# Performance work log

Hardware: AMD Instinct MI355X
Metric: run time of the kernel (lower is better)

Reference implementation:

```python
import jax, jax.numpy as jnp
import numpy as np

B = 8192
IN = 2048   # input_size
H = 2048    # hidden_size
D = IN + H  # combine feature dim = 4096


def setup_inputs() -> dict:
    key = jax.random.key(0)
    ks = jax.random.split(key, 11)
    s = 1.0 / np.sqrt(D)  # nn.Linear default init scale
    inp = {
        "input": jax.random.normal(ks[0], (B, D), jnp.float32),
        "hidden": jax.random.normal(ks[1], (B, D), jnp.float32),
        "cell": jax.random.normal(ks[2], (B, H), jnp.float32),
        "Wf": jax.random.uniform(ks[3], (D, H), jnp.float32, -s, s),
        "bf": jax.random.uniform(ks[4], (H,), jnp.float32, -s, s),
        "Wc": jax.random.uniform(ks[5], (D, H), jnp.float32, -s, s),
        "bc": jax.random.uniform(ks[6], (H,), jnp.float32, -s, s),
        "Wi": jax.random.uniform(ks[7], (D, H), jnp.float32, -s, s),
        "bi": jax.random.uniform(ks[8], (H,), jnp.float32, -s, s),
        "Wo": jax.random.uniform(ks[9], (D, H), jnp.float32, -s, s),
        "bo": jax.random.uniform(ks[10], (H,), jnp.float32, -s, s),
    }
    return inp


def reference(input, hidden, cell, Wf, bf, Wc, bc, Wi, bi, Wo, bo):
    combine = input + hidden  # [B, D] elementwise add (as in source, not concat)
    # Fuse the 4 gate GEMMs into one [D, 4H] GEMM for efficiency (same math).
    W = jnp.concatenate([Wf, Wc, Wi, Wo], axis=1)  # [D, 4H]
    b = jnp.concatenate([bf, bc, bi, bo])          # [4H]
    gates = combine @ W + b                        # [B, 4H]
    gf, gc, gi, go = jnp.split(gates, 4, axis=1)
    ft = jax.nn.sigmoid(gf)
    ct_ = jnp.tanh(gc)
    it = jax.nn.sigmoid(jax.nn.sigmoid(gi))  # double sigmoid, faithful to source
    cell_state = cell * ft + ct_ * it
    out = jax.nn.sigmoid(go)
    hidden_state = out * jnp.tanh(cell_state)
    return (out, hidden_state, cell_state)
```

## Files before the change

### kernel.cpp

```cpp
#include <hip/hip_runtime.h>
#include <hip/hip_bf16.h>

#define B_SZ 8192
#define D_SZ 4096
#define H_SZ 2048
#define N4H  8192
#define NT   (D_SZ / 64)

typedef __attribute__((ext_vector_type(8))) __bf16 bf16x8;
typedef __attribute__((ext_vector_type(4))) float f32x4;

#define GPTR(p) ((__attribute__((address_space(1))) void*)(p))
#define LPTR(p) ((__attribute__((address_space(3))) void*)(p))

__global__ void combine_k(const float* __restrict__ x, const float* __restrict__ h,
                          __hip_bfloat16* __restrict__ c) {
    const size_t n4 = (size_t)B_SZ * D_SZ / 4;
    const size_t stride = (size_t)gridDim.x * blockDim.x;
    for (size_t i = (size_t)blockIdx.x * blockDim.x + threadIdx.x; i < n4; i += stride) {
        float4 a = ((const float4*)x)[i];
        float4 b = ((const float4*)h)[i];
        short4 r;
        r.x = __builtin_bit_cast(short, __float2bfloat16(a.x + b.x));
        r.y = __builtin_bit_cast(short, __float2bfloat16(a.y + b.y));
        r.z = __builtin_bit_cast(short, __float2bfloat16(a.z + b.z));
        r.w = __builtin_bit_cast(short, __float2bfloat16(a.w + b.w));
        ((short4*)c)[i] = r;
    }
}

__global__ void transpose_w_k(const float* __restrict__ Wf, const float* __restrict__ Wc,
                              const float* __restrict__ Wi, const float* __restrict__ Wo,
                              __hip_bfloat16* __restrict__ WT) {
    __shared__ float t[32][33];
    const int k0 = blockIdx.x * 32;
    const int n0 = blockIdx.y * 32;
    const float* W = (n0 < H_SZ) ? Wf : (n0 < 2 * H_SZ) ? Wc : (n0 < 3 * H_SZ) ? Wi : Wo;
    const int nc = n0 & (H_SZ - 1);
    const int tx = threadIdx.x, ty = threadIdx.y;
#pragma unroll
    for (int j = 0; j < 4; ++j)
        t[ty + j * 8][tx] = W[(size_t)(k0 + ty + j * 8) * H_SZ + nc + tx];
    __syncthreads();
#pragma unroll
    for (int j = 0; j < 4; ++j)
        WT[(size_t)(n0 + ty + j * 8) * D_SZ + k0 + tx] = __float2bfloat16(t[tx][ty + j * 8]);
}


#define BAR()                                    \
    do {                                         \
        asm volatile("" ::: "memory");           \
        __builtin_amdgcn_s_barrier();            \
        asm volatile("" ::: "memory");           \
    } while (0)

#define STAGE(pbase, HSTRIDE, h, kt, region)                                           \
    do {                                                                               \
        __builtin_amdgcn_global_load_lds(                                              \
            GPTR((pbase) + (size_t)((h) * (HSTRIDE)) * D_SZ + (size_t)(kt) * 64),      \
            LPTR(smem + (region) + (h) * 16384 + wave * 1024), 16, 0, 0);              \
        __builtin_amdgcn_global_load_lds(                                              \
            GPTR((pbase) + (size_t)(128 + (h) * (HSTRIDE)) * D_SZ + (size_t)(kt) * 64),\
            LPTR(smem + (region) + (h) * 16384 + 8192 + wave * 1024), 16, 0, 0);       \
    } while (0)

#define LDA(dst, base, qm)                                                             \
    do {                                                                               \
        _Pragma("unroll") for (int mi = 0; mi < 4; ++mi) {                             \
            const int row_ = (qm) * 128 + wr * 64 + mi * 16 + fr;                      \
            dst[mi][0] = *(const bf16x8*)(smem + (base) + row_ * 128 + sw0);           \
            dst[mi][1] = *(const bf16x8*)(smem + (base) + row_ * 128 + sw1);           \
        }                                                                              \
    } while (0)

#define LDB(dst, base, qn)                                                             \
    do {                                                                               \
        _Pragma("unroll") for (int nf = 0; nf < 2; ++nf) {                             \
            const int row_ = (qn) * 128 + wc * 32 + nf * 16 + fr;                      \
            dst[nf][0] = *(const bf16x8*)(smem + (base) + row_ * 128 + sw0);           \
            dst[nf][1] = *(const bf16x8*)(smem + (base) + row_ * 128 + sw1);           \
        }                                                                              \
    } while (0)

#define MFMA_Q(qm, qn, areg, breg)                                                     \
    do {                                                                               \
        _Pragma("unroll") for (int mi = 0; mi < 4; ++mi)                               \
        _Pragma("unroll") for (int nf = 0; nf < 2; ++nf)                               \
        _Pragma("unroll") for (int ks = 0; ks < 2; ++ks)                               \
            acc[(qm) * 4 + mi][(qn) * 2 + nf] =                                        \
                __builtin_amdgcn_mfma_f32_16x16x32_bf16(                               \
                    areg[mi][ks], breg[nf][ks],                                        \
                    acc[(qm) * 4 + mi][(qn) * 2 + nf], 0, 0, 0);                       \
    } while (0)

__global__ __launch_bounds__(512, 2) void gemm8_k(
    const __hip_bfloat16* __restrict__ A,
    const __hip_bfloat16* __restrict__ BT,
    __hip_bfloat16* __restrict__ C)
{
    extern __shared__ char smem[];

    const int tid  = threadIdx.x;
    const int wave = tid >> 6;
    const int lane = tid & 63;
    const int wr = wave >> 2;
    const int wc = wave & 3;
    const int fr = lane & 15;
    const int sw0 = (((lane >> 4) + 0) ^ (fr & 7)) << 4;
    const int sw1 = (((lane >> 4) + 4) ^ (fr & 7)) << 4;

    const int wg = (blockIdx.x & 7) * 128 + (blockIdx.x >> 3);
    const int n0 = (wg & 31) * 256;
    const int m0 = (wg >> 5) * 256;

    const int r0   = tid >> 3;
    const int col0 = ((tid & 7) ^ (r0 & 7)) << 3;
    const __hip_bfloat16* pA = A  + (size_t)(m0 + r0) * D_SZ + col0;
    const __hip_bfloat16* pB = BT + (size_t)(n0 + ((r0 >> 5) << 6) + (r0 & 31)) * D_SZ + col0;

    f32x4 acc[8][4] = {};
    bf16x8 a[4][2], b0[2][2], b1[2][2];

    STAGE(pA, 64, 0, 0, 0);
    STAGE(pB, 32, 0, 0, 32768);
    STAGE(pA, 64, 1, 0, 0);
    STAGE(pB, 32, 1, 0, 32768);
    STAGE(pA, 64, 0, 1, 65536);
    STAGE(pB, 32, 0, 1, 98304);
    STAGE(pA, 64, 1, 1, 65536);
    asm volatile("s_waitcnt vmcnt(6)" ::: "memory");
    BAR();

    for (int t = 0; t < NT; ++t) {
        const int curA = (t & 1) * 65536;
        const int curB = curA + 32768;
        const int othB = (curA ^ 65536) + 32768;

        LDA(a, curA, 0);
        LDB(b0, curB, 0);
        if (t + 1 < NT) STAGE(pB, 32, 1, t + 1, othB);
        BAR();
        asm volatile("s_waitcnt lgkmcnt(0)" ::: "memory");
        __builtin_amdgcn_s_setprio(1);
        MFMA_Q(0, 0, a, b0);
        __builtin_amdgcn_s_setprio(0);
        BAR();

        LDB(b1, curB, 1);
        if (t + 2 < NT) STAGE(pA, 64, 0, t + 2, curA);
        BAR();
        asm volatile("s_waitcnt lgkmcnt(0)" ::: "memory");
        __builtin_amdgcn_s_setprio(1);
        MFMA_Q(0, 1, a, b1);
        __builtin_amdgcn_s_setprio(0);
        BAR();

        LDA(a, curA, 1);
        if (t + 2 < NT) STAGE(pB, 32, 0, t + 2, curB);
        BAR();
        asm volatile("s_waitcnt lgkmcnt(0)" ::: "memory");
        __builtin_amdgcn_s_setprio(1);
        MFMA_Q(1, 0, a, b0);
        __builtin_amdgcn_s_setprio(0);
        BAR();

        if (t + 2 < NT) STAGE(pA, 64, 1, t + 2, curA);
        BAR();
        __builtin_amdgcn_s_setprio(1);
        MFMA_Q(1, 1, a, b1);
        __builtin_amdgcn_s_setprio(0);
        if (t + 2 < NT) {
            asm volatile("s_waitcnt vmcnt(6)" ::: "memory");
        } else if (t + 1 < NT) {
            asm volatile("s_waitcnt vmcnt(0)" ::: "memory");
        }
        BAR();
    }

    const int crow = (lane >> 4) * 4;
    const int ccol = lane & 15;
#pragma unroll
    for (int ai = 0; ai < 8; ++ai)
#pragma unroll
        for (int bj = 0; bj < 4; ++bj) {
            const size_t base_r = (size_t)(m0 + wr * 128 + ai * 16 + crow);
            const size_t cidx   = (size_t)(n0 + wc * 64 + bj * 16 + ccol);
#pragma unroll
            for (int j = 0; j < 4; ++j)
                C[(base_r + j) * (size_t)N4H + cidx] = __float2bfloat16(acc[ai][bj][j]);
        }
}

__device__ __forceinline__ float bfbits(unsigned v, int j) {
    return __uint_as_float(j ? (v & 0xffff0000u) : (v << 16));
}
__device__ __forceinline__ float fsig(float x) { return 1.f / (1.f + __expf(-x)); }
__device__ __forceinline__ float ftanh(float x) {
    x = fminf(fmaxf(x, -15.f), 15.f);
    float e = __expf(2.f * x);
    return (e - 1.f) / (e + 1.f);
}

__global__ void gates_k(const __hip_bfloat16* __restrict__ g, const float* __restrict__ cell,
                        const float* __restrict__ bfb, const float* __restrict__ bcb,
                        const float* __restrict__ bib, const float* __restrict__ bob,
                        float* __restrict__ out) {
    const size_t BH = (size_t)B_SZ * H_SZ;
    float* hid = out + BH;
    float* cst = out + 2 * BH;
    const size_t n2 = BH / 2;
    const size_t stride = (size_t)gridDim.x * blockDim.x;
    for (size_t i = (size_t)blockIdx.x * blockDim.x + threadIdx.x; i < n2; i += stride) {
        const size_t e = i * 2;
        const int b = (int)(e >> 11);
        const int n = (int)(e & 2047);
        const unsigned* row = (const unsigned*)(g + (size_t)b * N4H);
        const unsigned vf = row[(n) >> 1];
        const unsigned vc = row[(n + 2048) >> 1];
        const unsigned vi = row[(n + 4096) >> 1];
        const unsigned vo = row[(n + 6144) >> 1];
        const float2 cl = *(const float2*)(cell + e);
        const float2 b_f = *(const float2*)(bfb + n);
        const float2 b_c = *(const float2*)(bcb + n);
        const float2 b_i = *(const float2*)(bib + n);
        const float2 b_o = *(const float2*)(bob + n);
        float r_out[2], r_hid[2], r_cst[2];
#pragma unroll
        for (int j = 0; j < 2; ++j) {
            const float gf = bfbits(vf, j) + (j ? b_f.y : b_f.x);
            const float gc = bfbits(vc, j) + (j ? b_c.y : b_c.x);
            const float gi = bfbits(vi, j) + (j ? b_i.y : b_i.x);
            const float go = bfbits(vo, j) + (j ? b_o.y : b_o.x);
            const float ft = fsig(gf);
            const float ct = ftanh(gc);
            const float it = fsig(fsig(gi));
            const float ot = fsig(go);
            const float cv = (j ? cl.y : cl.x);
            const float cs = cv * ft + ct * it;
            r_out[j] = ot;
            r_cst[j] = cs;
            r_hid[j] = ot * ftanh(cs);
        }
        *(float2*)(out + e) = make_float2(r_out[0], r_out[1]);
        *(float2*)(hid + e) = make_float2(r_hid[0], r_hid[1]);
        *(float2*)(cst + e) = make_float2(r_cst[0], r_cst[1]);
    }
}

extern "C" void kernel_launch(void* const* d_in, const int* in_sizes, int n_in,
                              void* d_out, int out_size, void* d_ws, size_t ws_size,
                              hipStream_t stream) {
    const float* input  = (const float*)d_in[0];
    const float* hidden = (const float*)d_in[1];
    const float* cell   = (const float*)d_in[2];
    const float* Wf     = (const float*)d_in[3];
    const float* bfb    = (const float*)d_in[4];
    const float* Wc     = (const float*)d_in[5];
    const float* bcb    = (const float*)d_in[6];
    const float* Wi     = (const float*)d_in[7];
    const float* bib    = (const float*)d_in[8];
    const float* Wo     = (const float*)d_in[9];
    const float* bob    = (const float*)d_in[10];
    float* out = (float*)d_out;

    char* ws = (char*)d_ws;
    __hip_bfloat16* comb  = (__hip_bfloat16*)ws;
    __hip_bfloat16* WT    = (__hip_bfloat16*)(ws + (size_t)B_SZ * D_SZ * 2);
    __hip_bfloat16* gates = (__hip_bfloat16*)(ws + (size_t)B_SZ * D_SZ * 2
                                                 + (size_t)N4H * D_SZ * 2);

    hipFuncSetAttribute(reinterpret_cast<const void*>(gemm8_k),
                        hipFuncAttributeMaxDynamicSharedMemorySize, 131072);

    combine_k<<<2048, 256, 0, stream>>>(input, hidden, comb);
    transpose_w_k<<<dim3(D_SZ / 32, N4H / 32), dim3(32, 8), 0, stream>>>(Wf, Wc, Wi, Wo, WT);
    gemm8_k<<<1024, 512, 131072, stream>>>(comb, WT, gates);
    gates_k<<<2048, 256, 0, stream>>>(gates, cell, bfb, bcb, bib, bob, out);
}
```

Baseline: 674.8 us.

## Fuse LSTM gate epilogue into GEMM via interleaved weight layout; merge prep kernels

The weight transpose now interleaves the four gates in groups of 16 columns, so each wave's 64-column tile holds the f/c/i/o values for the same 16 hidden units. That lets the GEMM epilogue apply the bias, activations and cell update directly from the accumulators, which removes the bf16 gates buffer round-trip and the separate gates kernel. The combine and transpose kernels are merged into one launch, nontemporal loads and stores are added, and the main loop is unrolled by two with constant buffer offsets. In exchange, the epilogue writes are scattered 4-byte stores and the cell reads are uncoalesced strided accesses, and the extra work may raise register pressure.

```diff
diff --git a/kernel.cpp b/kernel.cpp
--- a/kernel.cpp
+++ b/kernel.cpp
@@ -13,38 +13,46 @@
 #define GPTR(p) ((__attribute__((address_space(1))) void*)(p))
 #define LPTR(p) ((__attribute__((address_space(3))) void*)(p))
 
-__global__ void combine_k(const float* __restrict__ x, const float* __restrict__ h,
-                          __hip_bfloat16* __restrict__ c) {
-    const size_t n4 = (size_t)B_SZ * D_SZ / 4;
-    const size_t stride = (size_t)gridDim.x * blockDim.x;
-    for (size_t i = (size_t)blockIdx.x * blockDim.x + threadIdx.x; i < n4; i += stride) {
-        float4 a = ((const float4*)x)[i];
-        float4 b = ((const float4*)h)[i];
-        short4 r;
-        r.x = __builtin_bit_cast(short, __float2bfloat16(a.x + b.x));
-        r.y = __builtin_bit_cast(short, __float2bfloat16(a.y + b.y));
-        r.z = __builtin_bit_cast(short, __float2bfloat16(a.z + b.z));
-        r.w = __builtin_bit_cast(short, __float2bfloat16(a.w + b.w));
-        ((short4*)c)[i] = r;
-    }
-}
-
-__global__ void transpose_w_k(const float* __restrict__ Wf, const float* __restrict__ Wc,
-                              const float* __restrict__ Wi, const float* __restrict__ Wo,
-                              __hip_bfloat16* __restrict__ WT) {
+__global__ void prep_k(const float* __restrict__ x, const float* __restrict__ h,
+                       __hip_bfloat16* __restrict__ comb,
+                       const float* __restrict__ Wf, const float* __restrict__ Wc,
+                       const float* __restrict__ Wi, const float* __restrict__ Wo,
+                       __hip_bfloat16* __restrict__ WT) {
     __shared__ float t[32][33];
-    const int k0 = blockIdx.x * 32;
-    const int n0 = blockIdx.y * 32;
-    const float* W = (n0 < H_SZ) ? Wf : (n0 < 2 * H_SZ) ? Wc : (n0 < 3 * H_SZ) ? Wi : Wo;
-    const int nc = n0 & (H_SZ - 1);
-    const int tx = threadIdx.x, ty = threadIdx.y;
-#pragma unroll
-    for (int j = 0; j < 4; ++j)
-        t[ty + j * 8][tx] = W[(size_t)(k0 + ty + j * 8) * H_SZ + nc + tx];
-    __syncthreads();
-#pragma unroll
-    for (int j = 0; j < 4; ++j)
-        WT[(size_t)(n0 + ty + j * 8) * D_SZ + k0 + tx] = __float2bfloat16(t[tx][ty + j * 8]);
+    if (blockIdx.x < 2048) {
+        const size_t n4 = (size_t)B_SZ * D_SZ / 4;
+        const size_t stride = (size_t)2048 * 256;
+        for (size_t i = (size_t)blockIdx.x * 256 + threadIdx.x; i < n4; i += stride) {
+            f32x4 a = __builtin_nontemporal_load((const f32x4*)x + i);
+            f32x4 b = __builtin_nontemporal_load((const f32x4*)h + i);
+            short4 r;
+            r.x = __builtin_bit_cast(short, __float2bfloat16(a.x + b.x));
+            r.y = __builtin_bit_cast(short, __float2bfloat16(a.y + b.y));
+            r.z = __builtin_bit_cast(short, __float2bfloat16(a.z + b.z));
+            r.w = __builtin_bit_cast(short, __float2bfloat16(a.w + b.w));
+            ((short4*)comb)[i] = r;
+        }
+    } else {
+        const int b = blockIdx.x - 2048;
+        const int k0 = (b & 127) * 32;
+        const int n0 = (b >> 7) * 32;
+        const float* W = (n0 < H_SZ) ? Wf : (n0 < 2 * H_SZ) ? Wc
+                       : (n0 < 3 * H_SZ) ? Wi : Wo;
+        const int g = n0 >> 11;
+        const int nc = n0 & (H_SZ - 1);
+        const int tx = threadIdx.x & 31, ty = threadIdx.x >> 5;
+#pragma unroll
+        for (int j = 0; j < 4; ++j)
+            t[ty + j * 8][tx] = __builtin_nontemporal_load(
+                W + (size_t)(k0 + ty + j * 8) * H_SZ + nc + tx);
+        __syncthreads();
+#pragma unroll
+        for (int j = 0; j < 4; ++j) {
+            const int h2 = nc + ty + j * 8;
+            const int np = ((h2 >> 4) << 6) + (g << 4) + (h2 & 15);
+            WT[(size_t)np * D_SZ + k0 + tx] = __float2bfloat16(t[tx][ty + j * 8]);
+        }
+    }
 }
 
 
@@ -94,10 +102,64 @@
                     acc[(qm) * 4 + mi][(qn) * 2 + nf], 0, 0, 0);                       \
     } while (0)
 
+#define TILE(tcur, CA, CB, OB)                                                         \
+    {                                                                                  \
+                                                                  \
+        LDA(a, CA, 0);                                                                 \
+        LDB(b0, CB, 0);                                                                \
+        if ((tcur) + 1 < NT) STAGE(pB, 32, 1, (tcur) + 1, OB);                         \
+        BAR();                                                                         \
+        asm volatile("s_waitcnt lgkmcnt(0)" ::: "memory");                             \
+        __builtin_amdgcn_s_setprio(1);                                                 \
+        MFMA_Q(0, 0, a, b0);                                                           \
+        __builtin_amdgcn_s_setprio(0);                                                 \
+        BAR();                                                                         \
+                                                                  \
+        LDB(b1, CB, 1);                                                                \
+        if ((tcur) + 2 < NT) STAGE(pA, 64, 0, (tcur) + 2, CA);                         \
+        BAR();                                                                         \
+        asm volatile("s_waitcnt lgkmcnt(0)" ::: "memory");                             \
+        __builtin_amdgcn_s_setprio(1);                                                 \
+        MFMA_Q(0, 1, a, b1);                                                           \
+        __builtin_amdgcn_s_setprio(0);                                                 \
+        BAR();                                                                         \
+                                                                  \
+        LDA(a, CA, 1);                                                                 \
+        if ((tcur) + 2 < NT) STAGE(pB, 32, 0, (tcur) + 2, CB);                         \
+        BAR();                                                                         \
+        asm volatile("s_waitcnt lgkmcnt(0)" ::: "memory");                             \
+        __builtin_amdgcn_s_setprio(1);                                                 \
+        MFMA_Q(1, 0, a, b0);                                                           \
+        __builtin_amdgcn_s_setprio(0);                                                 \
+        BAR();                                                                         \
+                                                                  \
+        if ((tcur) + 2 < NT) STAGE(pA, 64, 1, (tcur) + 2, CA);                         \
+        BAR();                                                                         \
+        __builtin_amdgcn_s_setprio(1);                                                 \
+        MFMA_Q(1, 1, a, b1);                                                           \
+        __builtin_amdgcn_s_setprio(0);                                                 \
+        if ((tcur) + 2 < NT) {                                                         \
+            asm volatile("s_waitcnt vmcnt(6)" ::: "memory");                           \
+        } else if ((tcur) + 1 < NT) {                                                  \
+            asm volatile("s_waitcnt vmcnt(0)" ::: "memory");                           \
+        }                                                                              \
+        BAR();                                                                         \
+    }
+
+__device__ __forceinline__ float fsig(float x) { return 1.f / (1.f + __expf(-x)); }
+__device__ __forceinline__ float ftanh(float x) {
+    x = fminf(fmaxf(x, -15.f), 15.f);
+    float e = __expf(2.f * x);
+    return (e - 1.f) / (e + 1.f);
+}
+
 __global__ __launch_bounds__(512, 2) void gemm8_k(
     const __hip_bfloat16* __restrict__ A,
     const __hip_bfloat16* __restrict__ BT,
-    __hip_bfloat16* __restrict__ C)
+    const float* __restrict__ cell,
+    const float* __restrict__ bfb, const float* __restrict__ bcb,
+    const float* __restrict__ bib, const float* __restrict__ bob,
+    float* __restrict__ out)
 {
     extern __shared__ char smem[];
 
@@ -132,119 +194,38 @@
     asm volatile("s_waitcnt vmcnt(6)" ::: "memory");
     BAR();
 
-    for (int t = 0; t < NT; ++t) {
-        const int curA = (t & 1) * 65536;
-        const int curB = curA + 32768;
-        const int othB = (curA ^ 65536) + 32768;
-
-        LDA(a, curA, 0);
-        LDB(b0, curB, 0);
-        if (t + 1 < NT) STAGE(pB, 32, 1, t + 1, othB);
-        BAR();
-        asm volatile("s_waitcnt lgkmcnt(0)" ::: "memory");
-        __builtin_amdgcn_s_setprio(1);
-        MFMA_Q(0, 0, a, b0);
-        __builtin_amdgcn_s_setprio(0);
-        BAR();
-
-        LDB(b1, curB, 1);
-        if (t + 2 < NT) STAGE(pA, 64, 0, t + 2, curA);
-        BAR();
-        asm volatile("s_waitcnt lgkmcnt(0)" ::: "memory");
-        __builtin_amdgcn_s_setprio(1);
-        MFMA_Q(0, 1, a, b1);
-        __builtin_amdgcn_s_setprio(0);
-        BAR();
-
-        LDA(a, curA, 1);
-        if (t + 2 < NT) STAGE(pB, 32, 0, t + 2, curB);
-        BAR();
-        asm volatile("s_waitcnt lgkmcnt(0)" ::: "memory");
-        __builtin_amdgcn_s_setprio(1);
-        MFMA_Q(1, 0, a, b0);
-        __builtin_amdgcn_s_setprio(0);
-        BAR();
-
-        if (t + 2 < NT) STAGE(pA, 64, 1, t + 2, curA);
-        BAR();
-        __builtin_amdgcn_s_setprio(1);
-        MFMA_Q(1, 1, a, b1);
-        __builtin_amdgcn_s_setprio(0);
-        if (t + 2 < NT) {
-            asm volatile("s_waitcnt vmcnt(6)" ::: "memory");
-        } else if (t + 1 < NT) {
-            asm volatile("s_waitcnt vmcnt(0)" ::: "memory");
-        }
-        BAR();
+    for (int t = 0; t < NT; t += 2) {
+        TILE(t,     0,     32768, 98304);
+        TILE(t + 1, 65536, 98304, 32768);
     }
 
     const int crow = (lane >> 4) * 4;
     const int ccol = lane & 15;
-#pragma unroll
-    for (int ai = 0; ai < 8; ++ai)
-#pragma unroll
-        for (int bj = 0; bj < 4; ++bj) {
-            const size_t base_r = (size_t)(m0 + wr * 128 + ai * 16 + crow);
-            const size_t cidx   = (size_t)(n0 + wc * 64 + bj * 16 + ccol);
-#pragma unroll
-            for (int j = 0; j < 4; ++j)
-                C[(base_r + j) * (size_t)N4H + cidx] = __float2bfloat16(acc[ai][bj][j]);
-        }
-}
-
-__device__ __forceinline__ float bfbits(unsigned v, int j) {
-    return __uint_as_float(j ? (v & 0xffff0000u) : (v << 16));
-}
-__device__ __forceinline__ float fsig(float x) { return 1.f / (1.f + __expf(-x)); }
-__device__ __forceinline__ float ftanh(float x) {
-    x = fminf(fmaxf(x, -15.f), 15.f);
-    float e = __expf(2.f * x);
-    return (e - 1.f) / (e + 1.f);
-}
-
-__global__ void gates_k(const __hip_bfloat16* __restrict__ g, const float* __restrict__ cell,
-                        const float* __restrict__ bfb, const float* __restrict__ bcb,
-                        const float* __restrict__ bib, const float* __restrict__ bob,
-                        float* __restrict__ out) {
+    const int hh = (((n0 + wc * 64) >> 6) << 4) + ccol;
+    const float bf_ = bfb[hh], bc_ = bcb[hh], bi_ = bib[hh], bo_ = bob[hh];
     const size_t BH = (size_t)B_SZ * H_SZ;
-    float* hid = out + BH;
-    float* cst = out + 2 * BH;
-    const size_t n2 = BH / 2;
-    const size_t stride = (size_t)gridDim.x * blockDim.x;
-    for (size_t i = (size_t)blockIdx.x * blockDim.x + threadIdx.x; i < n2; i += stride) {
-        const size_t e = i * 2;
-        const int b = (int)(e >> 11);
-        const int n = (int)(e & 2047);
-        const unsigned* row = (const unsigned*)(g + (size_t)b * N4H);
-        const unsigned vf = row[(n) >> 1];
-        const unsigned vc = row[(n + 2048) >> 1];
-        const unsigned vi = row[(n + 4096) >> 1];
-        const unsigned vo = row[(n + 6144) >> 1];
-        const float2 cl = *(const float2*)(cell + e);
-        const float2 b_f = *(const float2*)(bfb + n);
-        const float2 b_c = *(const float2*)(bcb + n);
-        const float2 b_i = *(const float2*)(bib + n);
-        const float2 b_o = *(const float2*)(bob + n);
-        float r_out[2], r_hid[2], r_cst[2];
-#pragma unroll
-        for (int j = 0; j < 2; ++j) {
-            const float gf = bfbits(vf, j) + (j ? b_f.y : b_f.x);
-            const float gc = bfbits(vc, j) + (j ? b_c.y : b_c.x);
-            const float gi = bfbits(vi, j) + (j ? b_i.y : b_i.x);
-            const float go = bfbits(vo, j) + (j ? b_o.y : b_o.x);
+    float* hidp = out + BH;
+    float* cstp = out + 2 * BH;
+#pragma unroll
+    for (int ai = 0; ai < 8; ++ai) {
+#pragma unroll
+        for (int j = 0; j < 4; ++j) {
+            const size_t r = (size_t)(m0 + wr * 128 + ai * 16 + crow + j);
+            const size_t idx = r * H_SZ + hh;
+            const float gf = acc[ai][0][j] + bf_;
+            const float gc = acc[ai][1][j] + bc_;
+            const float gi = acc[ai][2][j] + bi_;
+            const float go = acc[ai][3][j] + bo_;
             const float ft = fsig(gf);
             const float ct = ftanh(gc);
             const float it = fsig(fsig(gi));
             const float ot = fsig(go);
-            const float cv = (j ? cl.y : cl.x);
+            const float cv = __builtin_nontemporal_load(cell + idx);
             const float cs = cv * ft + ct * it;
-            r_out[j] = ot;
-            r_cst[j] = cs;
-            r_hid[j] = ot * ftanh(cs);
+            __builtin_nontemporal_store(ot, out + idx);
+            __builtin_nontemporal_store(cs, cstp + idx);
+            __builtin_nontemporal_store(ot * ftanh(cs), hidp + idx);
         }
-        *(float2*)(out + e) = make_float2(r_out[0], r_out[1]);
-        *(float2*)(hid + e) = make_float2(r_hid[0], r_hid[1]);
-        *(float2*)(cst + e) = make_float2(r_cst[0], r_cst[1]);
     }
 }
 
@@ -265,16 +246,12 @@
     float* out = (float*)d_out;
 
     char* ws = (char*)d_ws;
-    __hip_bfloat16* comb  = (__hip_bfloat16*)ws;
-    __hip_bfloat16* WT    = (__hip_bfloat16*)(ws + (size_t)B_SZ * D_SZ * 2);
-    __hip_bfloat16* gates = (__hip_bfloat16*)(ws + (size_t)B_SZ * D_SZ * 2
-                                                 + (size_t)N4H * D_SZ * 2);
+    __hip_bfloat16* comb = (__hip_bfloat16*)ws;
+    __hip_bfloat16* WT   = (__hip_bfloat16*)(ws + (size_t)B_SZ * D_SZ * 2);
 
     hipFuncSetAttribute(reinterpret_cast<const void*>(gemm8_k),
                         hipFuncAttributeMaxDynamicSharedMemorySize, 131072);
 
-    combine_k<<<2048, 256, 0, stream>>>(input, hidden, comb);
-    transpose_w_k<<<dim3(D_SZ / 32, N4H / 32), dim3(32, 8), 0, stream>>>(Wf, Wc, Wi, Wo, WT);
-    gemm8_k<<<1024, 512, 131072, stream>>>(comb, WT, gates);
-    gates_k<<<2048, 256, 0, stream>>>(gates, cell, bfb, bcb, bib, bob, out);
-}
+    prep_k<<<2048 + 32768, 256, 0, stream>>>(input, hidden, comb, Wf, Wc, Wi, Wo, WT);
+    gemm8_k<<<1024, 512, 131072, stream>>>(comb, WT, cell, bfb, bcb, bib, bob, out);
+}
```

Result: faster. 630.6 us (-6.5%).
